# Kernel tuning notes

Measured on AMD Instinct MI355X. Metric: run time of the kernel, lower is better.

The kernel has to match this reference:

```python
import jax, jax.numpy as jnp
import numpy as np

B, S, D, H = 4, 2048, 1024, 16
DK = D // H


def setup_inputs() -> dict:
    key = jax.random.key(0)
    ks = jax.random.split(key, 11)
    std = 1.0 / np.sqrt(D)
    mk = lambda k: jax.random.uniform(k, (D, D), jnp.float32, -std, std)
    mb = lambda k: jax.random.uniform(k, (D,), jnp.float32, -std, std)
    return {
        "query": jax.random.normal(ks[0], (B, S, D), jnp.float32),
        "key": jax.random.normal(ks[1], (B, S, D), jnp.float32),
        "value": jax.random.normal(ks[2], (B, S, D), jnp.float32),
        "Wq": mk(ks[3]), "bq": mb(ks[4]),
        "Wk": mk(ks[5]), "bk": mb(ks[6]),
        "Wv": mk(ks[7]), "bv": mb(ks[8]),
        "Wo": mk(ks[9]), "bo": mb(ks[10]),
    }


def reference(query, key, value, Wq, bq, Wk, bk, Wv, bv, Wo, bo):
    # Linear projections (torch Linear: x @ W.T + b)
    Q = query @ Wq.T + bq   # [B,S,D]
    K = key @ Wk.T + bk
    V = value @ Wv.T + bv
    # split heads -> [B,H,S,DK]
    Q = Q.reshape(B, S, H, DK).transpose(0, 2, 1, 3)
    K = K.reshape(B, S, H, DK).transpose(0, 2, 1, 3)
    V = V.reshape(B, S, H, DK).transpose(0, 2, 1, 3)
    scale = 1.0 / jnp.sqrt(jnp.asarray(DK, Q.dtype))
    scores = jnp.einsum("bhqd,bhkd->bhqk", Q, K) * scale  # [B,H,S,S]
    attn = jax.nn.softmax(scores, axis=-1)
    out = jnp.einsum("bhqk,bhkd->bhqd", attn, V)          # [B,H,S,DK]
    out = out.transpose(0, 2, 1, 3).reshape(B, S, D)       # [B,S,D]
    return out @ Wo.T + bo
```

## Files before the change

### kernel.cpp

```cpp
#include <hip/hip_runtime.h>
#include <hip/hip_bf16.h>
#include <stdint.h>


using f32x4  = __attribute__((ext_vector_type(4))) float;
using f32x16 = __attribute__((ext_vector_type(16))) float;
using s16x8  = __attribute__((ext_vector_type(8))) short;
using u16x8  = __attribute__((ext_vector_type(8))) unsigned short;
using u16x4  = __attribute__((ext_vector_type(4))) unsigned short;

#define MFMA16(a, b, c) __builtin_amdgcn_mfma_f32_16x16x32_bf16((a), (b), (c), 0, 0, 0)
#define MFMA32(a, b, c) __builtin_amdgcn_mfma_f32_32x32x16_bf16((a), (b), (c), 0, 0, 0)

#define GLL16(gptr, lptr)                                                      \
  __builtin_amdgcn_global_load_lds(                                            \
      (const __attribute__((address_space(1))) void*)(gptr),                   \
      (__attribute__((address_space(3))) void*)(lptr), 16, 0, 0)

__device__ __forceinline__ unsigned short f2bf(float f) {
  union { __hip_bfloat16 h; unsigned short u; } cv;
  cv.h = __float2bfloat16(f);
  return cv.u;
}

__device__ __forceinline__ unsigned int pkrne(float a, float b) {
  unsigned int ua = __builtin_bit_cast(unsigned int, a);
  unsigned int ub = __builtin_bit_cast(unsigned int, b);
  ua = ua + 0x7FFFu + ((ua >> 16) & 1u);
  ub = ub + 0x7FFFu + ((ub >> 16) & 1u);
  return (ua >> 16) | (ub & 0xFFFF0000u);
}

__device__ __forceinline__ float exp2a(float x) {
  return __builtin_amdgcn_exp2f(x);
}

__global__ __launch_bounds__(256) void cast_all_kernel(
    const float* __restrict__ wq, const float* __restrict__ wk,
    const float* __restrict__ wv, const float* __restrict__ wo,
    const float* __restrict__ xq, const float* __restrict__ xk,
    const float* __restrict__ xv, unsigned short* __restrict__ wbf,
    unsigned short* __restrict__ oxq, unsigned short* __restrict__ oxk,
    unsigned short* __restrict__ oxv) {
  const int job = blockIdx.y;
  const int i = blockIdx.x * 256 + threadIdx.x;
  const float* src;
  unsigned short* dst;
  size_t off;
  if (job < 4) {
    src = (job == 0) ? wq : (job == 1) ? wk : (job == 2) ? wv : wo;
    dst = wbf + (size_t)job * 1048576;
    off = (size_t)i;
  } else {
    const int xi = job - 4, z = xi >> 3, sl = xi & 7;
    src = (z == 0) ? xq : (z == 1) ? xk : xv;
    dst = (z == 0) ? oxq : (z == 1) ? oxk : oxv;
    off = (size_t)sl * 262144 + i;
  }
  float4 f = reinterpret_cast<const float4*>(src)[off];
  uint2 p;
  p.x = pkrne(f.x, f.y);
  p.y = pkrne(f.z, f.w);
  *reinterpret_cast<uint2*>(dst + off * 4) = p;
}

__global__ __launch_bounds__(256) void gemm_qkv_kernel(
    const unsigned short* __restrict__ Xq, const unsigned short* __restrict__ Xk,
    const unsigned short* __restrict__ Xv, const unsigned short* __restrict__ wbf,
    const float* __restrict__ bq, const float* __restrict__ bk,
    const float* __restrict__ bv, unsigned short* __restrict__ Qh,
    unsigned short* __restrict__ Kh, unsigned short* __restrict__ Vh) {
  const int z = blockIdx.z;
  const unsigned short* Xbf = (z == 0) ? Xq : (z == 1) ? Xk : Xv;
  const unsigned short* W = wbf + (size_t)z * 1048576;
  const float* bias = (z == 0) ? bq : (z == 1) ? bk : bv;
  unsigned short* dst = (z == 0) ? Qh : (z == 1) ? Kh : Vh;
  const float qscale = (z == 0) ? 0.18033688011112042f : 1.0f;

  __shared__ __align__(16) unsigned short Asm_[128 * 64];
  __shared__ __align__(16) unsigned short Bsm_[128 * 64];

  const int t = threadIdx.x;
  const int lane = t & 63, w = t >> 6;
  const int g = lane >> 4, c = lane & 15;
  const int wm = (w >> 1) * 64, wn = (w & 1) * 64;
  const int n0 = (blockIdx.y & 7) * 128;
  const int m0 = (blockIdx.x * 8 + (blockIdx.y >> 3)) * 128;

  f32x4 acc[4][4];
#pragma unroll
  for (int i = 0; i < 4; i++)
#pragma unroll
    for (int j = 0; j < 4; j++) acc[i][j] = (f32x4)0.0f;

  const int blr = lane >> 3;
  const int bgc = (lane & 7) ^ blr;

  for (int kt = 0; kt < 16; ++kt) {
    const int k0 = kt * 64;
    __syncthreads();
#pragma unroll
    for (int i = 0; i < 4; i++) {
      int ii = w * 4 + i;
      const unsigned short* ga = Xbf + (size_t)(m0 + ii * 8 + blr) * 1024 + k0 + bgc * 8;
      GLL16(ga, &Asm_[ii * 512]);
      const unsigned short* gb = W + (size_t)(n0 + ii * 8 + blr) * 1024 + k0 + bgc * 8;
      GLL16(gb, &Bsm_[ii * 512]);
    }
    __syncthreads();

#pragma unroll
    for (int ks = 0; ks < 2; ks++) {
      s16x8 af[4], bfr[4];
#pragma unroll
      for (int mt = 0; mt < 4; mt++) {
        int r = wm + mt * 16 + c;
        af[mt] = *reinterpret_cast<const s16x8*>(&Asm_[r * 64 + (((ks * 4 + g) ^ (c & 7)) << 3)]);
      }
#pragma unroll
      for (int nt = 0; nt < 4; nt++) {
        int r = wn + nt * 16 + c;
        bfr[nt] = *reinterpret_cast<const s16x8*>(&Bsm_[r * 64 + (((ks * 4 + g) ^ (c & 7)) << 3)]);
      }
#pragma unroll
      for (int mt = 0; mt < 4; mt++)
#pragma unroll
        for (int nt = 0; nt < 4; nt++)
          acc[mt][nt] = MFMA16(af[mt], bfr[nt], acc[mt][nt]);
    }
  }

#pragma unroll
  for (int mt = 0; mt < 4; mt++)
#pragma unroll
    for (int nt = 0; nt < 4; nt++) {
      int n = n0 + wn + nt * 16 + c;
      float bb = bias[n];
      int h = n >> 6, dk = n & 63;
#pragma unroll
      for (int r = 0; r < 4; r++) {
        int m = m0 + wm + mt * 16 + g * 4 + r;
        int b = m >> 11, s = m & 2047;
        dst[(((size_t)b * 16 + h) * 2048 + s) * 64 + dk] =
            f2bf((acc[mt][nt][r] + bb) * qscale);
      }
    }
}

__global__ __launch_bounds__(256) void gemm_out_kernel(
    const unsigned short* __restrict__ AO, const unsigned short* __restrict__ Wo,
    const float* __restrict__ bo, float* __restrict__ out) {
  __shared__ __align__(16) unsigned short Asm_[128 * 64];
  __shared__ __align__(16) unsigned short Bsm_[64 * 64];

  const int t = threadIdx.x;
  const int lane = t & 63, w = t >> 6;
  const int g = lane >> 4, c = lane & 15;
  const int wm = (w >> 1) * 64, wn = (w & 1) * 32;
  const int n0 = (blockIdx.y & 15) * 64;
  const int m0 = (blockIdx.x * 8 + (blockIdx.y >> 4)) * 128;

  f32x4 acc[4][2];
#pragma unroll
  for (int i = 0; i < 4; i++)
#pragma unroll
    for (int j = 0; j < 2; j++) acc[i][j] = (f32x4)0.0f;

  const int blr = lane >> 3;
  const int bgc = (lane & 7) ^ blr;

  for (int kt = 0; kt < 16; ++kt) {
    const int k0 = kt * 64;
    __syncthreads();
#pragma unroll
    for (int i = 0; i < 4; i++) {
      int ii = w * 4 + i;
      const unsigned short* ga = AO + (size_t)(m0 + ii * 8 + blr) * 1024 + k0 + bgc * 8;
      GLL16(ga, &Asm_[ii * 512]);
    }
#pragma unroll
    for (int i = 0; i < 2; i++) {
      int ii = w * 2 + i;
      const unsigned short* gb = Wo + (size_t)(n0 + ii * 8 + blr) * 1024 + k0 + bgc * 8;
      GLL16(gb, &Bsm_[ii * 512]);
    }
    __syncthreads();

#pragma unroll
    for (int ks = 0; ks < 2; ks++) {
      s16x8 af[4], bfr[2];
#pragma unroll
      for (int mt = 0; mt < 4; mt++) {
        int r = wm + mt * 16 + c;
        af[mt] = *reinterpret_cast<const s16x8*>(&Asm_[r * 64 + (((ks * 4 + g) ^ (c & 7)) << 3)]);
      }
#pragma unroll
      for (int nt = 0; nt < 2; nt++) {
        int r = wn + nt * 16 + c;
        bfr[nt] = *reinterpret_cast<const s16x8*>(&Bsm_[r * 64 + (((ks * 4 + g) ^ (c & 7)) << 3)]);
      }
#pragma unroll
      for (int mt = 0; mt < 4; mt++)
#pragma unroll
        for (int nt = 0; nt < 2; nt++)
          acc[mt][nt] = MFMA16(af[mt], bfr[nt], acc[mt][nt]);
    }
  }

#pragma unroll
  for (int mt = 0; mt < 4; mt++)
#pragma unroll
    for (int nt = 0; nt < 2; nt++) {
      int n = n0 + wn + nt * 16 + c;
      float bb = bo[n];
#pragma unroll
      for (int r = 0; r < 4; r++) {
        int m = m0 + wm + mt * 16 + g * 4 + r;
        out[(size_t)m * 1024 + n] = acc[mt][nt][r] + bb;
      }
    }
}

__global__ __launch_bounds__(512) void attn_kernel(
    const unsigned short* __restrict__ Qh, const unsigned short* __restrict__ Kh,
    const unsigned short* __restrict__ Vh, unsigned short* __restrict__ AO) {
  const int bh = blockIdx.x * 8 + (blockIdx.y >> 3);
  const int b = bh >> 4, h = bh & 15;
  const int q0 = (blockIdx.y & 7) * 256;
  const int t = threadIdx.x, lane = t & 63, w = t >> 6;
  const int lo = lane & 31, hi = lane >> 5;

  __shared__ __align__(16) unsigned short Ks[2][64 * 64];
  __shared__ __align__(16) unsigned short Vt[2][64 * 64];

  const size_t kvbase = (size_t)bh * 2048 * 64;

  s16x8 qb[4];
  {
    const unsigned short* qp = Qh + kvbase + (size_t)(q0 + w * 32 + lo) * 64;
#pragma unroll
    for (int ks = 0; ks < 4; ks++)
      qb[ks] = *reinterpret_cast<const s16x8*>(qp + ks * 16 + hi * 8);
  }

  s16x8 onesb;
  {
    uint4 u;
    u.x = 0x3F803F80u; u.y = 0x3F803F80u; u.z = 0x3F803F80u; u.w = 0x3F803F80u;
    onesb = *reinterpret_cast<const s16x8*>(&u);
  }

  f32x16 oacc[2], lacc;
  oacc[0] = (f32x16)0.0f; oacc[1] = (f32x16)0.0f; lacc = (f32x16)0.0f;

  const int skrow = t >> 3, sks = t & 7;
  const int kgc = sks ^ (skrow & 7) ^ w;
  const int vkrow = t >> 3, vd0 = (t & 7) * 8;
  const int vwc = w ^ (t & 7);
  const int vcl = vkrow & 7;

  const int rx0 = (lo & 7) ^ (lo >> 3);
  const int rx1 = (lo & 7) ^ (4 | (lo >> 3));

  uint4 kk, vv;
  kk = *reinterpret_cast<const uint4*>(Kh + kvbase + (size_t)skrow * 64 + kgc * 8);
  vv = *reinterpret_cast<const uint4*>(Vh + kvbase + (size_t)vkrow * 64 + vd0);
  *reinterpret_cast<uint4*>(&Ks[0][(size_t)t * 8]) = kk;
  {
    const unsigned short* vs = reinterpret_cast<const unsigned short*>(&vv);
#pragma unroll
    for (int j = 0; j < 8; j++)
      Vt[0][(vd0 + j) * 64 + ((vwc ^ j) << 3) + vcl] = vs[j];
  }

  for (int it = 0; it < 32; ++it) {
    const int cur = it & 1, nxt = cur ^ 1;
    const bool more = (it < 31);
    if (more) {
      const int kv = (it + 1) * 64;
      kk = *reinterpret_cast<const uint4*>(Kh + kvbase + (size_t)(kv + skrow) * 64 + kgc * 8);
      vv = *reinterpret_cast<const uint4*>(Vh + kvbase + (size_t)(kv + vkrow) * 64 + vd0);
    }
    __syncthreads();

    f32x16 st[2];
    st[0] = (f32x16)0.0f; st[1] = (f32x16)0.0f;
#pragma unroll
    for (int kb = 0; kb < 2; kb++) {
      const int rx = kb ? rx1 : rx0;
#pragma unroll
      for (int ks = 0; ks < 4; ks++) {
        s16x8 ka = *reinterpret_cast<const s16x8*>(
            &Ks[cur][(kb * 32 + lo) * 64 + (((ks * 2 + hi) ^ rx) << 3)]);
        st[kb] = MFMA32(ka, qb[ks], st[kb]);
      }
    }

    s16x8 pa[4];
#pragma unroll
    for (int kb = 0; kb < 2; kb++) {
      float e[16];
#pragma unroll
      for (int r = 0; r < 16; r++) e[r] = exp2a(st[kb][r]);
#pragma unroll
      for (int half = 0; half < 2; half++) {
        const float* eb = e + half * 8;
        unsigned int x1 = pkrne(eb[0], eb[1]);
        unsigned int x2 = pkrne(eb[2], eb[3]);
        unsigned int y1 = pkrne(eb[4], eb[5]);
        unsigned int y2 = pkrne(eb[6], eb[7]);
        asm volatile("v_permlane32_swap_b32 %0, %1" : "+v"(x1), "+v"(y1));
        asm volatile("v_permlane32_swap_b32 %0, %1" : "+v"(x2), "+v"(y2));
        uint4 u;
        u.x = x1; u.y = x2; u.z = y1; u.w = y2;
        pa[kb * 2 + half] = *reinterpret_cast<const s16x8*>(&u);
      }
    }

#pragma unroll
    for (int ks = 0; ks < 4; ks++) lacc = MFMA32(pa[ks], onesb, lacc);

    if (more) {
      *reinterpret_cast<uint4*>(&Ks[nxt][(size_t)t * 8]) = kk;
      const unsigned short* vs = reinterpret_cast<const unsigned short*>(&vv);
#pragma unroll
      for (int j = 0; j < 8; j++)
        Vt[nxt][(vd0 + j) * 64 + ((vwc ^ j) << 3) + vcl] = vs[j];
    }

#pragma unroll
    for (int ks = 0; ks < 4; ks++)
#pragma unroll
      for (int db = 0; db < 2; db++) {
        const int rx = db ? rx1 : rx0;
        s16x8 vb = *reinterpret_cast<const s16x8*>(
            &Vt[cur][(db * 32 + lo) * 64 + (((ks * 2 + hi) ^ rx) << 3)]);
        oacc[db] = MFMA32(pa[ks], vb, oacc[db]);
      }
  }

#pragma unroll
  for (int r = 0; r < 16; r++) {
    float inv_r = 1.0f / lacc[r];
    int qr = (r & 3) + ((r >> 2) << 3) + (hi << 2);
    int srow = q0 + w * 32 + qr;
    size_t obase = ((size_t)b * 2048 + srow) * 1024 + (size_t)h * 64;
    AO[obase + lo]      = f2bf(oacc[0][r] * inv_r);
    AO[obase + 32 + lo] = f2bf(oacc[1][r] * inv_r);
  }
}

extern "C" void kernel_launch(void* const* d_in, const int* in_sizes, int n_in,
                              void* d_out, int out_size, void* d_ws, size_t ws_size,
                              hipStream_t stream) {
  const float* query = (const float*)d_in[0];
  const float* key   = (const float*)d_in[1];
  const float* value = (const float*)d_in[2];
  const float* Wq = (const float*)d_in[3];
  const float* bq = (const float*)d_in[4];
  const float* Wk = (const float*)d_in[5];
  const float* bk = (const float*)d_in[6];
  const float* Wv = (const float*)d_in[7];
  const float* bv = (const float*)d_in[8];
  const float* Wo = (const float*)d_in[9];
  const float* bo = (const float*)d_in[10];

  uint8_t* wsb = (uint8_t*)d_ws;
  unsigned short* wbf = (unsigned short*)wsb;
  unsigned short* Qh  = (unsigned short*)(wsb + 8388608);
  unsigned short* Kh  = (unsigned short*)(wsb + 8388608 + 16777216);
  unsigned short* Vh  = (unsigned short*)(wsb + 8388608 + 2 * 16777216);
  unsigned short* AO  = (unsigned short*)(wsb + 8388608 + 3 * 16777216);
  unsigned short* Xq = AO;
  unsigned short* Xk = (unsigned short*)d_out;
  unsigned short* Xv = (unsigned short*)d_out + 8388608;

  cast_all_kernel<<<dim3(1024, 28), dim3(256), 0, stream>>>(
      Wq, Wk, Wv, Wo, query, key, value, wbf, Xq, Xk, Xv);
  gemm_qkv_kernel<<<dim3(8, 64, 3), dim3(256), 0, stream>>>(
      Xq, Xk, Xv, wbf, bq, bk, bv, Qh, Kh, Vh);
  attn_kernel<<<dim3(8, 64), dim3(512), 0, stream>>>(Qh, Kh, Vh, AO);
  gemm_out_kernel<<<dim3(8, 128), dim3(256), 0, stream>>>(
      AO, wbf + (size_t)3 * 1048576, bo, (float*)d_out);
}
```

Before: 220.7 us.

## Emit V pre-transposed from projection GEMM and stream K/V via direct-to-LDS loads

A separate V projection kernel computes the transposed product and writes V as [b,h,dk,s], so attention no longer transposes V through scalar LDS stores. The attention kernel now loads K and V tiles with global_load_lds directly into double-buffered shared memory, with one barrier per iteration instead of staging through registers. The bf16 pack helper also uses a single byte-permute instruction. In exchange there is an extra kernel launch, and the V epilogue writes scattered 2-byte values along the sequence stride.

```diff
diff --git a/kernel.cpp b/kernel.cpp
--- a/kernel.cpp
+++ b/kernel.cpp
@@ -28,7 +28,7 @@
   unsigned int ub = __builtin_bit_cast(unsigned int, b);
   ua = ua + 0x7FFFu + ((ua >> 16) & 1u);
   ub = ub + 0x7FFFu + ((ub >> 16) & 1u);
-  return (ua >> 16) | (ub & 0xFFFF0000u);
+  return __builtin_amdgcn_perm(ub, ua, 0x07060302u);
 }
 
 __device__ __forceinline__ float exp2a(float x) {
@@ -66,15 +66,14 @@
 
 __global__ __launch_bounds__(256) void gemm_qkv_kernel(
     const unsigned short* __restrict__ Xq, const unsigned short* __restrict__ Xk,
-    const unsigned short* __restrict__ Xv, const unsigned short* __restrict__ wbf,
+    const unsigned short* __restrict__ wbf,
     const float* __restrict__ bq, const float* __restrict__ bk,
-    const float* __restrict__ bv, unsigned short* __restrict__ Qh,
-    unsigned short* __restrict__ Kh, unsigned short* __restrict__ Vh) {
+    unsigned short* __restrict__ Qh, unsigned short* __restrict__ Kh) {
   const int z = blockIdx.z;
-  const unsigned short* Xbf = (z == 0) ? Xq : (z == 1) ? Xk : Xv;
+  const unsigned short* Xbf = (z == 0) ? Xq : Xk;
   const unsigned short* W = wbf + (size_t)z * 1048576;
-  const float* bias = (z == 0) ? bq : (z == 1) ? bk : bv;
-  unsigned short* dst = (z == 0) ? Qh : (z == 1) ? Kh : Vh;
+  const float* bias = (z == 0) ? bq : bk;
+  unsigned short* dst = (z == 0) ? Qh : Kh;
   const float qscale = (z == 0) ? 0.18033688011112042f : 1.0f;
 
   __shared__ __align__(16) unsigned short Asm_[128 * 64];
@@ -143,6 +142,80 @@
         int b = m >> 11, s = m & 2047;
         dst[(((size_t)b * 16 + h) * 2048 + s) * 64 + dk] =
             f2bf((acc[mt][nt][r] + bb) * qscale);
+      }
+    }
+}
+
+__global__ __launch_bounds__(256) void gemm_v_kernel(
+    const unsigned short* __restrict__ Xv, const unsigned short* __restrict__ wbf,
+    const float* __restrict__ bv, unsigned short* __restrict__ Vh) {
+  const unsigned short* W = wbf + (size_t)2 * 1048576;
+
+  __shared__ __align__(16) unsigned short Asm_[128 * 64];
+  __shared__ __align__(16) unsigned short Bsm_[128 * 64];
+
+  const int t = threadIdx.x;
+  const int lane = t & 63, w = t >> 6;
+  const int g = lane >> 4, c = lane & 15;
+  const int wm = (w >> 1) * 64, wn = (w & 1) * 64;
+  const int n0 = (blockIdx.y & 7) * 128;
+  const int m0 = (blockIdx.x * 8 + (blockIdx.y >> 3)) * 128;
+
+  f32x4 acc[4][4];
+#pragma unroll
+  for (int i = 0; i < 4; i++)
+#pragma unroll
+    for (int j = 0; j < 4; j++) acc[i][j] = (f32x4)0.0f;
+
+  const int blr = lane >> 3;
+  const int bgc = (lane & 7) ^ blr;
+
+  for (int kt = 0; kt < 16; ++kt) {
+    const int k0 = kt * 64;
+    __syncthreads();
+#pragma unroll
+    for (int i = 0; i < 4; i++) {
+      int ii = w * 4 + i;
+      const unsigned short* ga = Xv + (size_t)(m0 + ii * 8 + blr) * 1024 + k0 + bgc * 8;
+      GLL16(ga, &Asm_[ii * 512]);
+      const unsigned short* gb = W + (size_t)(n0 + ii * 8 + blr) * 1024 + k0 + bgc * 8;
+      GLL16(gb, &Bsm_[ii * 512]);
+    }
+    __syncthreads();
+
+#pragma unroll
+    for (int ks = 0; ks < 2; ks++) {
+      s16x8 af[4], bfr[4];
+#pragma unroll
+      for (int mt = 0; mt < 4; mt++) {
+        int r = wm + mt * 16 + c;
+        af[mt] = *reinterpret_cast<const s16x8*>(&Asm_[r * 64 + (((ks * 4 + g) ^ (c & 7)) << 3)]);
+      }
+#pragma unroll
+      for (int nt = 0; nt < 4; nt++) {
+        int r = wn + nt * 16 + c;
+        bfr[nt] = *reinterpret_cast<const s16x8*>(&Bsm_[r * 64 + (((ks * 4 + g) ^ (c & 7)) << 3)]);
+      }
+#pragma unroll
+      for (int nt = 0; nt < 4; nt++)
+#pragma unroll
+        for (int mt = 0; mt < 4; mt++)
+          acc[nt][mt] = MFMA16(bfr[nt], af[mt], acc[nt][mt]);
+    }
+  }
+
+#pragma unroll
+  for (int nt = 0; nt < 4; nt++)
+#pragma unroll
+    for (int mt = 0; mt < 4; mt++) {
+      int m = m0 + wm + mt * 16 + c;
+      int b = m >> 11, s = m & 2047;
+#pragma unroll
+      for (int r = 0; r < 4; r++) {
+        int n = n0 + wn + nt * 16 + g * 4 + r;
+        int h = n >> 6, dk = n & 63;
+        Vh[(((size_t)b * 16 + h) * 64 + dk) * 2048 + s] =
+            f2bf(acc[nt][mt][r] + bv[n]);
       }
     }
 }
@@ -231,7 +304,7 @@
   const int lo = lane & 31, hi = lane >> 5;
 
   __shared__ __align__(16) unsigned short Ks[2][64 * 64];
-  __shared__ __align__(16) unsigned short Vt[2][64 * 64];
+  __shared__ __align__(16) unsigned short Vs[2][64 * 64];
 
   const size_t kvbase = (size_t)bh * 2048 * 64;
 
@@ -253,35 +326,25 @@
   f32x16 oacc[2], lacc;
   oacc[0] = (f32x16)0.0f; oacc[1] = (f32x16)0.0f; lacc = (f32x16)0.0f;
 
-  const int skrow = t >> 3, sks = t & 7;
-  const int kgc = sks ^ (skrow & 7) ^ w;
-  const int vkrow = t >> 3, vd0 = (t & 7) * 8;
-  const int vwc = w ^ (t & 7);
-  const int vcl = vkrow & 7;
+  const int srow = t >> 3;
+  const int gch = (t & 7) ^ (srow & 7) ^ w;
+  const unsigned short* Kg = Kh + kvbase + (size_t)srow * 64 + gch * 8;
+  const unsigned short* Vg = Vh + kvbase + (size_t)srow * 2048 + gch * 8;
 
   const int rx0 = (lo & 7) ^ (lo >> 3);
   const int rx1 = (lo & 7) ^ (4 | (lo >> 3));
 
-  uint4 kk, vv;
-  kk = *reinterpret_cast<const uint4*>(Kh + kvbase + (size_t)skrow * 64 + kgc * 8);
-  vv = *reinterpret_cast<const uint4*>(Vh + kvbase + (size_t)vkrow * 64 + vd0);
-  *reinterpret_cast<uint4*>(&Ks[0][(size_t)t * 8]) = kk;
-  {
-    const unsigned short* vs = reinterpret_cast<const unsigned short*>(&vv);
-#pragma unroll
-    for (int j = 0; j < 8; j++)
-      Vt[0][(vd0 + j) * 64 + ((vwc ^ j) << 3) + vcl] = vs[j];
-  }
+  GLL16(Kg, &Ks[0][w * 512]);
+  GLL16(Vg, &Vs[0][w * 512]);
+  __syncthreads();
 
   for (int it = 0; it < 32; ++it) {
-    const int cur = it & 1, nxt = cur ^ 1;
-    const bool more = (it < 31);
-    if (more) {
+    const int cur = it & 1;
+    if (it < 31) {
       const int kv = (it + 1) * 64;
-      kk = *reinterpret_cast<const uint4*>(Kh + kvbase + (size_t)(kv + skrow) * 64 + kgc * 8);
-      vv = *reinterpret_cast<const uint4*>(Vh + kvbase + (size_t)(kv + vkrow) * 64 + vd0);
-    }
-    __syncthreads();
+      GLL16(Kg + (size_t)kv * 64, &Ks[cur ^ 1][w * 512]);
+      GLL16(Vg + kv, &Vs[cur ^ 1][w * 512]);
+    }
 
     f32x16 st[2];
     st[0] = (f32x16)0.0f; st[1] = (f32x16)0.0f;
@@ -320,31 +383,25 @@
 #pragma unroll
     for (int ks = 0; ks < 4; ks++) lacc = MFMA32(pa[ks], onesb, lacc);
 
-    if (more) {
-      *reinterpret_cast<uint4*>(&Ks[nxt][(size_t)t * 8]) = kk;
-      const unsigned short* vs = reinterpret_cast<const unsigned short*>(&vv);
-#pragma unroll
-      for (int j = 0; j < 8; j++)
-        Vt[nxt][(vd0 + j) * 64 + ((vwc ^ j) << 3) + vcl] = vs[j];
-    }
-
 #pragma unroll
     for (int ks = 0; ks < 4; ks++)
 #pragma unroll
       for (int db = 0; db < 2; db++) {
         const int rx = db ? rx1 : rx0;
         s16x8 vb = *reinterpret_cast<const s16x8*>(
-            &Vt[cur][(db * 32 + lo) * 64 + (((ks * 2 + hi) ^ rx) << 3)]);
+            &Vs[cur][(db * 32 + lo) * 64 + (((ks * 2 + hi) ^ rx) << 3)]);
         oacc[db] = MFMA32(pa[ks], vb, oacc[db]);
       }
+
+    __syncthreads();
   }
 
 #pragma unroll
   for (int r = 0; r < 16; r++) {
     float inv_r = 1.0f / lacc[r];
     int qr = (r & 3) + ((r >> 2) << 3) + (hi << 2);
-    int srow = q0 + w * 32 + qr;
-    size_t obase = ((size_t)b * 2048 + srow) * 1024 + (size_t)h * 64;
+    int srow_q = q0 + w * 32 + qr;
+    size_t obase = ((size_t)b * 2048 + srow_q) * 1024 + (size_t)h * 64;
     AO[obase + lo]      = f2bf(oacc[0][r] * inv_r);
     AO[obase + 32 + lo] = f2bf(oacc[1][r] * inv_r);
   }
@@ -377,8 +434,9 @@
 
   cast_all_kernel<<<dim3(1024, 28), dim3(256), 0, stream>>>(
       Wq, Wk, Wv, Wo, query, key, value, wbf, Xq, Xk, Xv);
-  gemm_qkv_kernel<<<dim3(8, 64, 3), dim3(256), 0, stream>>>(
-      Xq, Xk, Xv, wbf, bq, bk, bv, Qh, Kh, Vh);
+  gemm_qkv_kernel<<<dim3(8, 64, 2), dim3(256), 0, stream>>>(
+      Xq, Xk, wbf, bq, bk, Qh, Kh);
+  gemm_v_kernel<<<dim3(8, 64), dim3(256), 0, stream>>>(Xv, wbf, bv, Vh);
   attn_kernel<<<dim3(8, 64), dim3(512), 0, stream>>>(Qh, Kh, Vh, AO);
   gemm_out_kernel<<<dim3(8, 128), dim3(256), 0, stream>>>(
       AO, wbf + (size_t)3 * 1048576, bo, (float*)d_out);
```

Result: no change. 217.9 us (-1.3%).

## Store V transposed from QKV GEMM and software-pipeline attention with async LDS loads

Applied to the files above, without the earlier changes.

The QKV projection now writes V in a transposed [b,h,dk,s] layout by swapping MFMA operands for the V slice, so the attention kernel no longer has to transpose V through scalar LDS stores. Attention switches to a triple-buffered pipeline that uses global_load_lds for K and V and overlaps the next tile's QK^T and softmax with the current tile's PV. The bf16 pack also uses a single byte-permute instruction. This costs more LDS (three buffers) and scattered 2-byte stores in the V epilogue of the GEMM.

```diff
diff --git a/kernel.cpp b/kernel.cpp
--- a/kernel.cpp
+++ b/kernel.cpp
@@ -28,7 +28,7 @@
   unsigned int ub = __builtin_bit_cast(unsigned int, b);
   ua = ua + 0x7FFFu + ((ua >> 16) & 1u);
   ub = ub + 0x7FFFu + ((ub >> 16) & 1u);
-  return (ua >> 16) | (ub & 0xFFFF0000u);
+  return __builtin_amdgcn_perm(ub, ua, 0x07060302u);
 }
 
 __device__ __forceinline__ float exp2a(float x) {
@@ -64,7 +64,7 @@
   *reinterpret_cast<uint2*>(dst + off * 4) = p;
 }
 
-__global__ __launch_bounds__(256) void gemm_qkv_kernel(
+__global__ __launch_bounds__(256) void gemm_qkvv_kernel(
     const unsigned short* __restrict__ Xq, const unsigned short* __restrict__ Xk,
     const unsigned short* __restrict__ Xv, const unsigned short* __restrict__ wbf,
     const float* __restrict__ bq, const float* __restrict__ bk,
@@ -74,7 +74,6 @@
   const unsigned short* Xbf = (z == 0) ? Xq : (z == 1) ? Xk : Xv;
   const unsigned short* W = wbf + (size_t)z * 1048576;
   const float* bias = (z == 0) ? bq : (z == 1) ? bk : bv;
-  unsigned short* dst = (z == 0) ? Qh : (z == 1) ? Kh : Vh;
   const float qscale = (z == 0) ? 0.18033688011112042f : 1.0f;
 
   __shared__ __align__(16) unsigned short Asm_[128 * 64];
@@ -122,29 +121,55 @@
         int r = wn + nt * 16 + c;
         bfr[nt] = *reinterpret_cast<const s16x8*>(&Bsm_[r * 64 + (((ks * 4 + g) ^ (c & 7)) << 3)]);
       }
-#pragma unroll
-      for (int mt = 0; mt < 4; mt++)
+      if (z == 2) {
 #pragma unroll
         for (int nt = 0; nt < 4; nt++)
-          acc[mt][nt] = MFMA16(af[mt], bfr[nt], acc[mt][nt]);
-    }
-  }
-
-#pragma unroll
-  for (int mt = 0; mt < 4; mt++)
-#pragma unroll
-    for (int nt = 0; nt < 4; nt++) {
-      int n = n0 + wn + nt * 16 + c;
-      float bb = bias[n];
-      int h = n >> 6, dk = n & 63;
-#pragma unroll
-      for (int r = 0; r < 4; r++) {
-        int m = m0 + wm + mt * 16 + g * 4 + r;
+#pragma unroll
+          for (int mt = 0; mt < 4; mt++)
+            acc[nt][mt] = MFMA16(bfr[nt], af[mt], acc[nt][mt]);
+      } else {
+#pragma unroll
+        for (int mt = 0; mt < 4; mt++)
+#pragma unroll
+          for (int nt = 0; nt < 4; nt++)
+            acc[mt][nt] = MFMA16(af[mt], bfr[nt], acc[mt][nt]);
+      }
+    }
+  }
+
+  if (z == 2) {
+#pragma unroll
+    for (int nt = 0; nt < 4; nt++)
+#pragma unroll
+      for (int mt = 0; mt < 4; mt++) {
+        int m = m0 + wm + mt * 16 + c;
         int b = m >> 11, s = m & 2047;
-        dst[(((size_t)b * 16 + h) * 2048 + s) * 64 + dk] =
-            f2bf((acc[mt][nt][r] + bb) * qscale);
-      }
-    }
+#pragma unroll
+        for (int r = 0; r < 4; r++) {
+          int n = n0 + wn + nt * 16 + g * 4 + r;
+          int h = n >> 6, dk = n & 63;
+          Vh[(((size_t)b * 16 + h) * 64 + dk) * 2048 + s] =
+              f2bf(acc[nt][mt][r] + bv[n]);
+        }
+      }
+  } else {
+    unsigned short* dst = (z == 0) ? Qh : Kh;
+#pragma unroll
+    for (int mt = 0; mt < 4; mt++)
+#pragma unroll
+      for (int nt = 0; nt < 4; nt++) {
+        int n = n0 + wn + nt * 16 + c;
+        float bb = bias[n];
+        int h = n >> 6, dk = n & 63;
+#pragma unroll
+        for (int r = 0; r < 4; r++) {
+          int m = m0 + wm + mt * 16 + g * 4 + r;
+          int b = m >> 11, s = m & 2047;
+          dst[(((size_t)b * 16 + h) * 2048 + s) * 64 + dk] =
+              f2bf((acc[mt][nt][r] + bb) * qscale);
+        }
+      }
+  }
 }
 
 __global__ __launch_bounds__(256) void gemm_out_kernel(
@@ -230,8 +255,8 @@
   const int t = threadIdx.x, lane = t & 63, w = t >> 6;
   const int lo = lane & 31, hi = lane >> 5;
 
-  __shared__ __align__(16) unsigned short Ks[2][64 * 64];
-  __shared__ __align__(16) unsigned short Vt[2][64 * 64];
+  __shared__ __align__(16) unsigned short Ks[3][64 * 64];
+  __shared__ __align__(16) unsigned short Vs[3][64 * 64];
 
   const size_t kvbase = (size_t)bh * 2048 * 64;
 
@@ -253,37 +278,19 @@
   f32x16 oacc[2], lacc;
   oacc[0] = (f32x16)0.0f; oacc[1] = (f32x16)0.0f; lacc = (f32x16)0.0f;
 
-  const int skrow = t >> 3, sks = t & 7;
-  const int kgc = sks ^ (skrow & 7) ^ w;
-  const int vkrow = t >> 3, vd0 = (t & 7) * 8;
-  const int vwc = w ^ (t & 7);
-  const int vcl = vkrow & 7;
+  const int srow = t >> 3;
+  const int gch = (t & 7) ^ (srow & 7) ^ w;
+  const unsigned short* Kg = Kh + kvbase + (size_t)srow * 64 + gch * 8;
+  const unsigned short* Vg = Vh + kvbase + (size_t)srow * 2048 + gch * 8;
 
   const int rx0 = (lo & 7) ^ (lo >> 3);
   const int rx1 = (lo & 7) ^ (4 | (lo >> 3));
 
-  uint4 kk, vv;
-  kk = *reinterpret_cast<const uint4*>(Kh + kvbase + (size_t)skrow * 64 + kgc * 8);
-  vv = *reinterpret_cast<const uint4*>(Vh + kvbase + (size_t)vkrow * 64 + vd0);
-  *reinterpret_cast<uint4*>(&Ks[0][(size_t)t * 8]) = kk;
-  {
-    const unsigned short* vs = reinterpret_cast<const unsigned short*>(&vv);
-#pragma unroll
-    for (int j = 0; j < 8; j++)
-      Vt[0][(vd0 + j) * 64 + ((vwc ^ j) << 3) + vcl] = vs[j];
-  }
-
-  for (int it = 0; it < 32; ++it) {
-    const int cur = it & 1, nxt = cur ^ 1;
-    const bool more = (it < 31);
-    if (more) {
-      const int kv = (it + 1) * 64;
-      kk = *reinterpret_cast<const uint4*>(Kh + kvbase + (size_t)(kv + skrow) * 64 + kgc * 8);
-      vv = *reinterpret_cast<const uint4*>(Vh + kvbase + (size_t)(kv + vkrow) * 64 + vd0);
-    }
-    __syncthreads();
-
-    f32x16 st[2];
+  auto stage = [&](int buf, int tile) {
+    GLL16(Kg + (size_t)tile * 4096, &Ks[buf][w * 512]);
+    GLL16(Vg + tile * 64, &Vs[buf][w * 512]);
+  };
+  auto qk_tile = [&](int buf, f32x16* st) {
     st[0] = (f32x16)0.0f; st[1] = (f32x16)0.0f;
 #pragma unroll
     for (int kb = 0; kb < 2; kb++) {
@@ -291,12 +298,12 @@
 #pragma unroll
       for (int ks = 0; ks < 4; ks++) {
         s16x8 ka = *reinterpret_cast<const s16x8*>(
-            &Ks[cur][(kb * 32 + lo) * 64 + (((ks * 2 + hi) ^ rx) << 3)]);
+            &Ks[buf][(kb * 32 + lo) * 64 + (((ks * 2 + hi) ^ rx) << 3)]);
         st[kb] = MFMA32(ka, qb[ks], st[kb]);
       }
     }
-
-    s16x8 pa[4];
+  };
+  auto sm_pack = [&](const f32x16* st, s16x8* pa) {
 #pragma unroll
     for (int kb = 0; kb < 2; kb++) {
       float e[16];
@@ -316,35 +323,63 @@
         pa[kb * 2 + half] = *reinterpret_cast<const s16x8*>(&u);
       }
     }
-
+  };
+  auto pv_tile = [&](int buf, const s16x8* pa) {
 #pragma unroll
     for (int ks = 0; ks < 4; ks++) lacc = MFMA32(pa[ks], onesb, lacc);
-
-    if (more) {
-      *reinterpret_cast<uint4*>(&Ks[nxt][(size_t)t * 8]) = kk;
-      const unsigned short* vs = reinterpret_cast<const unsigned short*>(&vv);
-#pragma unroll
-      for (int j = 0; j < 8; j++)
-        Vt[nxt][(vd0 + j) * 64 + ((vwc ^ j) << 3) + vcl] = vs[j];
-    }
-
 #pragma unroll
     for (int ks = 0; ks < 4; ks++)
 #pragma unroll
       for (int db = 0; db < 2; db++) {
         const int rx = db ? rx1 : rx0;
         s16x8 vb = *reinterpret_cast<const s16x8*>(
-            &Vt[cur][(db * 32 + lo) * 64 + (((ks * 2 + hi) ^ rx) << 3)]);
+            &Vs[buf][(db * 32 + lo) * 64 + (((ks * 2 + hi) ^ rx) << 3)]);
         oacc[db] = MFMA32(pa[ks], vb, oacc[db]);
       }
+  };
+
+  s16x8 paA[4], paB[4];
+
+  stage(0, 0);
+  __syncthreads();
+  stage(1, 1);
+  {
+    f32x16 st0[2];
+    qk_tile(0, st0);
+    sm_pack(st0, paA);
+  }
+  __syncthreads();
+
+  for (int u = 0; u < 16; ++u) {
+    const int te = 2 * u;
+    if (te + 2 < 32) stage((te + 2) % 3, te + 2);
+    {
+      f32x16 stn[2];
+      qk_tile((te + 1) % 3, stn);
+      pv_tile(te % 3, paA);
+      sm_pack(stn, paB);
+    }
+    __syncthreads();
+
+    const int to = te + 1;
+    if (to + 2 < 32) stage((to + 2) % 3, to + 2);
+    if (to + 1 < 32) {
+      f32x16 stn[2];
+      qk_tile((to + 1) % 3, stn);
+      pv_tile(to % 3, paB);
+      sm_pack(stn, paA);
+    } else {
+      pv_tile(to % 3, paB);
+    }
+    __syncthreads();
   }
 
 #pragma unroll
   for (int r = 0; r < 16; r++) {
     float inv_r = 1.0f / lacc[r];
     int qr = (r & 3) + ((r >> 2) << 3) + (hi << 2);
-    int srow = q0 + w * 32 + qr;
-    size_t obase = ((size_t)b * 2048 + srow) * 1024 + (size_t)h * 64;
+    int srow_q = q0 + w * 32 + qr;
+    size_t obase = ((size_t)b * 2048 + srow_q) * 1024 + (size_t)h * 64;
     AO[obase + lo]      = f2bf(oacc[0][r] * inv_r);
     AO[obase + 32 + lo] = f2bf(oacc[1][r] * inv_r);
   }
@@ -377,7 +412,7 @@
 
   cast_all_kernel<<<dim3(1024, 28), dim3(256), 0, stream>>>(
       Wq, Wk, Wv, Wo, query, key, value, wbf, Xq, Xk, Xv);
-  gemm_qkv_kernel<<<dim3(8, 64, 3), dim3(256), 0, stream>>>(
+  gemm_qkvv_kernel<<<dim3(8, 64, 3), dim3(256), 0, stream>>>(
       Xq, Xk, Xv, wbf, bq, bk, bv, Qh, Kh, Vh);
   attn_kernel<<<dim3(8, 64), dim3(512), 0, stream>>>(Qh, Kh, Vh, AO);
   gemm_out_kernel<<<dim3(8, 128), dim3(256), 0, stream>>>(
```

After: 230.0 us. 1.04x slower.
